# Kernel optimization log

Measured on AMD Instinct MI355X. Metric: run time of the kernel, lower is better.

Reference implementation:

```python
import jax, jax.numpy as jnp
import numpy as np

TIME_SHIFT_OFFSET = 288
NOTE_OFF_OFFSET = 128
VELOCITY_OFFSET = 256
MAX_REL_POS = 25
MAX_REL_TIME = 200
MAX_REL_PITCH = 128


def _last_true_pos(flag):
    # flag: (B,T) bool -> (B,T) index of most recent True at or before each position, -1 if none
    B, T = flag.shape
    pos = jnp.where(flag, jnp.arange(T)[None, :], -1)
    return jax.lax.cummax(pos, axis=1)


def time_rel_idx(tok):
    # Faithful vectorization of Head.relative_time index computation.
    B, T = tok.shape
    is_t = tok >= TIME_SHIFT_OFFSET
    vals = jnp.where(is_t, tok - TIME_SHIFT_OFFSET, 0)
    abs_t = (jnp.cumsum(vals, axis=1) + 1).astype(jnp.float32)
    last = _last_true_pos(is_t)
    cur = jnp.where(last >= 0, jnp.take_along_axis(abs_t, jnp.maximum(last, 0), axis=1), jnp.nan)
    prop = jnp.round(cur / 10.0)  # (B,T), NaN before first time token
    dist = prop[:, None, :] - prop[:, :, None]  # [b,i,j] = prop[j]-prop[i]
    idx = jnp.clip(dist, -MAX_REL_TIME, MAX_REL_TIME) + MAX_REL_TIME
    return jnp.where(jnp.isnan(idx), 0.0, idx).astype(jnp.int32)  # (B,T,T)


def pitch_rel_idx(tok):
    # Per the reference loop, note values are also written one step ahead (i-1,i,i+1),
    # so position j ends up with the note value known after step min(j+1, T-1).
    B, T = tok.shape
    is_n = tok < VELOCITY_OFFSET
    vals = (jnp.where(tok >= NOTE_OFF_OFFSET, tok - NOTE_OFF_OFFSET, tok) + 1).astype(jnp.float32)
    last = _last_true_pos(is_n)
    ff = jnp.where(last >= 0, jnp.take_along_axis(vals, jnp.maximum(last, 0), axis=1), jnp.nan)
    prop = ff[:, jnp.minimum(jnp.arange(T) + 1, T - 1)]
    dist = prop[:, None, :] - prop[:, :, None]
    idx = jnp.clip(dist, -MAX_REL_PITCH, MAX_REL_PITCH) + MAX_REL_PITCH
    return jnp.where(jnp.isnan(idx), 0.0, idx).astype(jnp.int32)  # (B,T,T)


def setup_inputs() -> dict:
    key = jax.random.key(0)
    ks = jax.random.split(key, 12)
    B, T, C, H = 2, 512, 512, 64
    x = jax.random.normal(ks[0], (B, T, C), dtype=jnp.float32)
    token_batch = jax.random.randint(ks[1], (B, T), 0, 388)
    s = C ** -0.5
    Wk = jax.random.normal(ks[2], (C, H), dtype=jnp.float32) * s
    Wq = jax.random.normal(ks[3], (C, H), dtype=jnp.float32) * s
    Wv = jax.random.normal(ks[4], (C, H), dtype=jnp.float32) * s
    e = 0.02
    Ek_pos = jax.random.normal(ks[5], (2 * MAX_REL_POS + 1, H), dtype=jnp.float32) * e
    Ev_pos = jax.random.normal(ks[6], (2 * MAX_REL_POS + 1, H), dtype=jnp.float32) * e
    Ek_time = jax.random.normal(ks[7], (2 * MAX_REL_TIME + 1, H), dtype=jnp.float32) * e
    Ev_time = jax.random.normal(ks[8], (2 * MAX_REL_TIME + 1, H), dtype=jnp.float32) * e
    Ek_pitch = jax.random.normal(ks[9], (2 * MAX_REL_PITCH + 1, H), dtype=jnp.float32) * e
    Ev_pitch = jax.random.normal(ks[10], (2 * MAX_REL_PITCH + 1, H), dtype=jnp.float32) * e
    return dict(x=x, token_batch=token_batch, Wk=Wk, Wq=Wq, Wv=Wv,
                Ek_pos=Ek_pos, Ev_pos=Ev_pos, Ek_time=Ek_time, Ev_time=Ev_time,
                Ek_pitch=Ek_pitch, Ev_pitch=Ev_pitch)


def reference(x, token_batch, Wk, Wq, Wv, Ek_pos, Ev_pos, Ek_time, Ev_time, Ek_pitch, Ev_pitch):
    B, T, C = x.shape
    q = x @ Wq  # (B,T,H)
    k = x @ Wk
    v = x @ Wv
    wei = jnp.einsum('btc,bsc->bts', q, k) * (C ** -0.5)  # (B,T,T), scaled by n_embd per source
    pos = jnp.arange(T)
    pd = jnp.clip(pos[None, :] - pos[:, None], -MAX_REL_POS, MAX_REL_POS) + MAX_REL_POS  # (T,T)
    tidx = time_rel_idx(token_batch)
    nidx = pitch_rel_idx(token_batch)
    # Note: the source einsums sum the relative embeddings over i as well (btj output).
    wei = wei + jnp.einsum('ijc,btc->btj', Ek_pos[pd], q)
    wei = wei + jnp.einsum('bijc,btc->btj', Ek_time[tidx], q)
    wei = wei + jnp.einsum('bijc,btc->btj', Ek_pitch[nidx], q)
    causal = jnp.tril(jnp.ones((T, T), dtype=bool))
    wei = jnp.where(causal[None], wei, -jnp.inf)
    wei = jax.nn.softmax(wei, axis=-1)  # dropout p=0.0
    out = wei @ v
    out = out + jnp.einsum('ijc,btj->btc', Ev_pos[pd], wei)
    out = out + jnp.einsum('bijc,btj->btc', Ev_time[tidx], wei)
    out = out + jnp.einsum('bijc,btj->btc', Ev_pitch[nidx], wei)
    return out
```

## Files before the change

kernel.cpp:

```cpp
#include <hip/hip_runtime.h>
#include <math.h>

#define B 2
#define T 512
#define C 512
#define H 64

#define SCALE 0.044194173824159216f

static __device__ __forceinline__ float qnan() { return __builtin_nanf(""); }

__global__ __launch_bounds__(64) void scan_kernel(const int* __restrict__ tok,
                                                  float* __restrict__ prop_t,
                                                  float* __restrict__ prop_p,
                                                  int* __restrict__ cntP,
                                                  int* __restrict__ meta,
                                                  float* __restrict__ tval,
                                                  int* __restrict__ tcnt) {
    int b = blockIdx.x;
    int lane = threadIdx.x;
    const int* tb = tok + b * T;

    __shared__ int tks[T];
    __shared__ float ptv[T];
    __shared__ float ff[T];
    __shared__ int hist[129];
    __shared__ int cnts[520];
    __shared__ int nanPc;

    for (int i = lane; i < T; i += 64) tks[i] = tb[i];
    for (int i = lane; i < 520; i += 64) cnts[i] = 0;
    for (int i = lane; i < 129; i += 64) hist[i] = 0;
    if (lane == 0) nanPc = 0;
    __syncthreads();

    const int p0 = lane * 8;
    unsigned long long lowmask = lane ? ((1ull << lane) - 1ull) : 0ull;

    {
        float lsum[8];
        bool lflag[8];
        float s = 0.f;
        bool f = false;
#pragma unroll
        for (int i = 0; i < 8; ++i) {
            int tk = tks[p0 + i];
            if (tk >= 288) { s += (float)(tk - 288); f = true; }
            lsum[i] = s;
            lflag[i] = f;
        }
        float inc = s;
#pragma unroll
        for (int off = 1; off < 64; off <<= 1) {
            float o = __shfl_up(inc, off);
            if (lane >= off) inc += o;
        }
        float ex = inc - s;
        unsigned long long fmask = __ballot(f);
        bool exf = (fmask & lowmask) != 0ull;
#pragma unroll
        for (int i = 0; i < 8; ++i) {
            bool have = exf | lflag[i];
            float outv = have ? rintf((ex + lsum[i] + 1.0f) / 10.0f) : qnan();
            prop_t[b * T + p0 + i] = outv;
            ptv[p0 + i] = outv;
        }
    }

    {
        float lval[8];
        bool lvalid[8];
        float cv = 0.f;
        bool cvd = false;
#pragma unroll
        for (int i = 0; i < 8; ++i) {
            int tk = tks[p0 + i];
            if (tk < 256) {
                cv = (float)((tk >= 128 ? tk - 128 : tk) + 1);
                cvd = true;
            }
            lval[i] = cv;
            lvalid[i] = cvd;
        }
        unsigned long long vmask = __ballot(cvd);
        unsigned long long lower = vmask & lowmask;
        bool exvd = lower != 0ull;
        int src = 63 - __clzll(lower | 1ull);
        float exv = __shfl(cv, src);
#pragma unroll
        for (int i = 0; i < 8; ++i) {
            bool hv = exvd | lvalid[i];
            float fv = lvalid[i] ? lval[i] : exv;
            ff[p0 + i] = hv ? fv : qnan();
        }
    }
    __syncthreads();

    for (int i = lane; i < T; i += 64) {
        float v = ff[min(i + 1, T - 1)];
        prop_p[b * T + i] = v;
        if (v == v) atomicAdd(&hist[(int)v - 1], 1);
        else atomicAdd(&nanPc, 1);
    }

    int lstart[8];
    int lcnt = 0, lnan = 0;
#pragma unroll
    for (int u = 0; u < 8; ++u) {
        int i = p0 + u;
        float cur = ptv[i];
        bool val = (cur == cur);
        bool st = false;
        if (val) {
            if (i == 0) st = true;
            else {
                float pv = ptv[i - 1];
                st = !(pv == pv) || (pv != cur);
            }
        } else lnan++;
        lstart[u] = st;
        lcnt += st;
    }
    int incs = lcnt;
#pragma unroll
    for (int off = 1; off < 64; off <<= 1) {
        int o = __shfl_up(incs, off);
        if (lane >= off) incs += o;
    }
    int base = incs - lcnt;
    int Lruns = __shfl(incs, 63);
    int tn = lnan;
#pragma unroll
    for (int off = 32; off; off >>= 1) tn += __shfl_down(tn, off);
    tn = __shfl(tn, 0);

    int s2 = base;
#pragma unroll
    for (int u = 0; u < 8; ++u) {
        int i = p0 + u;
        float cur = ptv[i];
        if (lstart[u]) { tval[b * 520 + s2] = cur; s2++; }
        if (cur == cur) atomicAdd(&cnts[s2 - 1], 1);
    }
    __syncthreads();

    for (int i = lane; i < Lruns; i += 64) tcnt[b * 520 + i] = cnts[i];
    for (int i = lane; i < 129; i += 64) cntP[b * 129 + i] = hist[i];
    if (lane == 0) {
        meta[b * 4] = Lruns;
        meta[b * 4 + 1] = tn;
        meta[b * 4 + 2] = nanPc;
    }
}

__global__ __launch_bounds__(256) void qkv_kernel(const float* __restrict__ x,
                                                  const float* __restrict__ Wq,
                                                  const float* __restrict__ Wk,
                                                  const float* __restrict__ Wv,
                                                  float* __restrict__ q,
                                                  float* __restrict__ k,
                                                  float* __restrict__ v) {
    int rg = blockIdx.x & 255;
    int m = blockIdx.x >> 8;
    int tid = threadIdx.x;
    int wave = tid >> 6;
    int lane = tid & 63;
    int g = lane >> 4;
    int c4 = lane & 15;

    const float* Wm = (m == 0) ? Wq : ((m == 1) ? Wk : Wv);
    float* Om = (m == 0) ? q : ((m == 1) ? k : v);

    __shared__ float xs[4 * C];
    const float4* xv4 = (const float4*)(x + (size_t)rg * 4 * C);
    float4* xs4 = (float4*)xs;
    xs4[tid] = xv4[tid];
    xs4[tid + 256] = xv4[tid + 256];
    __syncthreads();

    const float4* W4 = (const float4*)Wm;
    const float* xr = xs + wave * C;

    float4 acc = make_float4(0.f, 0.f, 0.f, 0.f);
#pragma unroll 8
    for (int u = 0; u < 128; ++u) {
        int kk = u * 4 + g;
        float4 w4 = W4[kk * 16 + c4];
        float xv = xr[kk];
        acc.x = fmaf(xv, w4.x, acc.x);
        acc.y = fmaf(xv, w4.y, acc.y);
        acc.z = fmaf(xv, w4.z, acc.z);
        acc.w = fmaf(xv, w4.w, acc.w);
    }

#pragma unroll
    for (int mask = 16; mask <= 32; mask <<= 1) {
        acc.x += __shfl_xor(acc.x, mask);
        acc.y += __shfl_xor(acc.y, mask);
        acc.z += __shfl_xor(acc.z, mask);
        acc.w += __shfl_xor(acc.w, mask);
    }

    if (g == 0) {
        float4* orow = (float4*)(Om + (size_t)(rg * 4 + wave) * H);
        orow[c4] = acc;
    }
}

__global__ __launch_bounds__(256) void relsum_kernel(
    const float* __restrict__ prop_t, const float* __restrict__ prop_p,
    const int* __restrict__ cntP, const int* __restrict__ meta,
    const float* __restrict__ tval, const int* __restrict__ tcnt,
    const float* __restrict__ Ek_pos, const float* __restrict__ Ev_pos,
    const float* __restrict__ Ek_time, const float* __restrict__ Ev_time,
    const float* __restrict__ Ek_pitch, const float* __restrict__ Ev_pitch,
    float* __restrict__ k, float* __restrict__ v) {
    int b = blockIdx.x >> 9;
    int j = blockIdx.x & 511;
    int tid = threadIdx.x;
    int wave = tid >> 6;
    int c = tid & 63;

    __shared__ float tvL[520];
    __shared__ int tcL[520];
    __shared__ int cpL[129];
    __shared__ float redK[256];
    __shared__ float redV[256];

    int L = meta[b * 4];
    int nanT = meta[b * 4 + 1];
    int nanP = meta[b * 4 + 2];
    for (int i = tid; i < L; i += 256) {
        tvL[i] = tval[b * 520 + i];
        tcL[i] = tcnt[b * 520 + i];
    }
    if (tid < 129) cpL[tid] = cntP[b * 129 + tid];
    __syncthreads();

    float pjt = prop_t[b * T + j];
    float pjp = prop_p[b * T + j];

    float aK = 0.f, aV = 0.f;

    int NE = 130 + L + 1;
    for (int e = wave; e < NE; e += 4) {
        int idx, cnt;
        const float* EK;
        const float* EV;
        if (e < 130) {
            EK = Ek_pitch; EV = Ev_pitch;
            if (e == 129) { idx = 0; cnt = nanP; }
            else {
                cnt = cpL[e];
                float dv = pjp - (float)(e + 1);
                idx = (dv != dv) ? 0 : (int)dv + 128;
            }
        } else {
            EK = Ek_time; EV = Ev_time;
            int r = e - 130;
            if (r == L) { idx = 0; cnt = nanT; }
            else {
                cnt = tcL[r];
                float dt = pjt - tvL[r];
                idx = (dt != dt) ? 0 : (int)fminf(fmaxf(dt, -200.f), 200.f) + 200;
            }
        }
        if (cnt) {
            float fc = (float)cnt;
            aK = fmaf(fc, EK[idx * H + c], aK);
            aV = fmaf(fc, EV[idx * H + c], aV);
        }
    }

    int lo = max(-25, j - (T - 1));
    int hi = min(25, j);
    for (int d = lo + wave; d <= hi; d += 4) {
        aK += Ek_pos[(d + 25) * H + c];
        aV += Ev_pos[(d + 25) * H + c];
    }
    if (wave == 0) {
        float c50 = (float)max(j - 25, 0);
        float c0 = (float)max((T - 26) - j, 0);
        aK = fmaf(c50, Ek_pos[50 * H + c], aK);
        aK = fmaf(c0, Ek_pos[0 * H + c], aK);
        aV = fmaf(c50, Ev_pos[50 * H + c], aV);
        aV = fmaf(c0, Ev_pos[0 * H + c], aV);
    }

    redK[tid] = aK;
    redV[tid] = aV;
    __syncthreads();

    if (tid < 64) {
        float sK = redK[tid] + redK[64 + tid] + redK[128 + tid] + redK[192 + tid];
        float sV = redV[tid] + redV[64 + tid] + redV[128 + tid] + redV[192 + tid];
        size_t o = (size_t)blockIdx.x * H + tid;
        k[o] = SCALE * k[o] + sK;
        v[o] = v[o] + sV;
    }
}

__global__ __launch_bounds__(256) void attn_kernel(const float* __restrict__ q,
                                                   const float* __restrict__ kp,
                                                   const float* __restrict__ vp,
                                                   float* __restrict__ out) {
    int b = blockIdx.x >> 7;
    int g = blockIdx.x & 127;
    int tid = threadIdx.x;
    int wave = tid >> 6;
    int lane = tid & 63;

    int t = (wave < 2) ? (2 * g + wave) : (511 - 2 * g - (wave - 2));
    int ns = t + 1;

    __shared__ float kt[64 * 65];
    __shared__ float vt[64 * 64];
    __shared__ float qs[4][64];
    __shared__ float pS[4][64];

    qs[wave][lane] = q[((size_t)b * T + t) * H + lane];

    const float* kb = kp + (size_t)b * T * H;
    const float* vb = vp + (size_t)b * T * H;
    int ntiles = (512 - 2 * g + 63) / 64;

    float m = -INFINITY;
    float l = 0.f;
    float acc = 0.f;

    for (int it = 0; it < ntiles; ++it) {
        int s0 = it * 64;

#pragma unroll
        for (int i = 0; i < 4; ++i) {
            int f = i * 256 + tid;
            int r = f >> 4;
            int c0 = (f & 15) << 2;
            int sr = min(s0 + r, T - 1);
            const float4 kv = *(const float4*)(kb + (size_t)sr * H + c0);
            const float4 vv = *(const float4*)(vb + (size_t)sr * H + c0);
            kt[r * 65 + c0 + 0] = kv.x;
            kt[r * 65 + c0 + 1] = kv.y;
            kt[r * 65 + c0 + 2] = kv.z;
            kt[r * 65 + c0 + 3] = kv.w;
            *(float4*)(vt + r * 64 + c0) = vv;
        }
        __syncthreads();

        if (s0 < ns) {
            int s = s0 + lane;
            float sc = -INFINITY;
            if (s < ns) {
                float d = 0.f;
                const float* kr = kt + lane * 65;
                const float* qw = qs[wave];
#pragma unroll
                for (int c = 0; c < 64; ++c) d = fmaf(qw[c], kr[c], d);
                sc = d;
            }
            float mt = sc;
#pragma unroll
            for (int off = 32; off; off >>= 1) mt = fmaxf(mt, __shfl_xor(mt, off));
            float mnew = fmaxf(m, mt);
            float alpha = __expf(m - mnew);
            float p = (s < ns) ? __expf(sc - mnew) : 0.f;
            l = l * alpha + p;
            pS[wave][lane] = p;
            m = mnew;

            float a = 0.f;
            int smax = min(64, ns - s0);
            for (int ss = 0; ss < smax; ++ss)
                a = fmaf(pS[wave][ss], vt[ss * 64 + lane], a);
            acc = acc * alpha + a;
        }
        __syncthreads();
    }

    float lt = l;
#pragma unroll
    for (int off = 32; off; off >>= 1) lt += __shfl_xor(lt, off);

    out[((size_t)b * T + t) * H + lane] = acc / lt;
}

extern "C" void kernel_launch(void* const* d_in, const int* in_sizes, int n_in,
                              void* d_out, int out_size, void* d_ws, size_t ws_size,
                              hipStream_t stream) {
    const float* x        = (const float*)d_in[0];
    const int*   tok      = (const int*)d_in[1];
    const float* Wk       = (const float*)d_in[2];
    const float* Wq       = (const float*)d_in[3];
    const float* Wv       = (const float*)d_in[4];
    const float* Ek_pos   = (const float*)d_in[5];
    const float* Ev_pos   = (const float*)d_in[6];
    const float* Ek_time  = (const float*)d_in[7];
    const float* Ev_time  = (const float*)d_in[8];
    const float* Ek_pitch = (const float*)d_in[9];
    const float* Ev_pitch = (const float*)d_in[10];
    float* out = (float*)d_out;

    float* ws = (float*)d_ws;
    float* q      = ws;
    float* k      = q + B * T * H;
    float* v      = k + B * T * H;
    float* prop_t = v + B * T * H;
    float* prop_p = prop_t + B * T;
    int*   cntP   = (int*)(prop_p + B * T);
    int*   meta   = cntP + B * 129;
    float* tval   = (float*)(meta + B * 4);
    int*   tcnt   = (int*)(tval + B * 520);

    scan_kernel<<<B, 64, 0, stream>>>(tok, prop_t, prop_p, cntP, meta, tval, tcnt);
    qkv_kernel<<<3 * 256, 256, 0, stream>>>(x, Wq, Wk, Wv, q, k, v);
    relsum_kernel<<<B * T, 256, 0, stream>>>(prop_t, prop_p, cntP, meta, tval, tcnt,
                                             Ek_pos, Ev_pos, Ek_time, Ev_time,
                                             Ek_pitch, Ev_pitch, k, v);
    attn_kernel<<<B * 128, 256, 0, stream>>>(q, k, v, out);
}
```

Baseline: 137.2 us.

## Register-block QKV projection, split relsum loops, and add ILP accumulators in attention

The QKV kernel now has each wave compute four rows at once, so every weight load is reused four times, and it launches a quarter as many blocks. The relsum kernel splits the mixed pitch/time loop into two separate loops with simpler index math and fewer branches. The attention kernel's dot-product and PV accumulations use four independent accumulators to break serial FMA dependency chains. In exchange, register pressure and shared memory per QKV block go up, fewer QKV blocks may leave parts of the GPU idle, and the changed summation order gives slightly different floating-point results.

New measurement: 131.0 us. 4.5% less time.

```diff
diff --git a/kernel.cpp b/kernel.cpp
--- a/kernel.cpp
+++ b/kernel.cpp
@@ -160,8 +160,8 @@
                                                   float* __restrict__ q,
                                                   float* __restrict__ k,
                                                   float* __restrict__ v) {
-    int rg = blockIdx.x & 255;
-    int m = blockIdx.x >> 8;
+    int rg = blockIdx.x & 63;
+    int m = blockIdx.x >> 6;
     int tid = threadIdx.x;
     int wave = tid >> 6;
     int lane = tid & 63;
@@ -171,39 +171,54 @@
     const float* Wm = (m == 0) ? Wq : ((m == 1) ? Wk : Wv);
     float* Om = (m == 0) ? q : ((m == 1) ? k : v);
 
-    __shared__ float xs[4 * C];
-    const float4* xv4 = (const float4*)(x + (size_t)rg * 4 * C);
+    __shared__ float xs[16 * C];
+    const float4* xv4 = (const float4*)(x + (size_t)rg * 16 * C);
     float4* xs4 = (float4*)xs;
-    xs4[tid] = xv4[tid];
-    xs4[tid + 256] = xv4[tid + 256];
+#pragma unroll
+    for (int i = 0; i < 8; ++i) xs4[tid + 256 * i] = xv4[tid + 256 * i];
     __syncthreads();
 
     const float4* W4 = (const float4*)Wm;
-    const float* xr = xs + wave * C;
-
-    float4 acc = make_float4(0.f, 0.f, 0.f, 0.f);
-#pragma unroll 8
+    const float* xr = xs + (wave * 4) * C;
+
+    float4 a0 = make_float4(0.f, 0.f, 0.f, 0.f);
+    float4 a1 = a0, a2 = a0, a3 = a0;
+#pragma unroll 4
     for (int u = 0; u < 128; ++u) {
         int kk = u * 4 + g;
         float4 w4 = W4[kk * 16 + c4];
-        float xv = xr[kk];
-        acc.x = fmaf(xv, w4.x, acc.x);
-        acc.y = fmaf(xv, w4.y, acc.y);
-        acc.z = fmaf(xv, w4.z, acc.z);
-        acc.w = fmaf(xv, w4.w, acc.w);
+        float x0 = xr[kk];
+        float x1 = xr[C + kk];
+        float x2 = xr[2 * C + kk];
+        float x3 = xr[3 * C + kk];
+        a0.x = fmaf(x0, w4.x, a0.x); a0.y = fmaf(x0, w4.y, a0.y);
+        a0.z = fmaf(x0, w4.z, a0.z); a0.w = fmaf(x0, w4.w, a0.w);
+        a1.x = fmaf(x1, w4.x, a1.x); a1.y = fmaf(x1, w4.y, a1.y);
+        a1.z = fmaf(x1, w4.z, a1.z); a1.w = fmaf(x1, w4.w, a1.w);
+        a2.x = fmaf(x2, w4.x, a2.x); a2.y = fmaf(x2, w4.y, a2.y);
+        a2.z = fmaf(x2, w4.z, a2.z); a2.w = fmaf(x2, w4.w, a2.w);
+        a3.x = fmaf(x3, w4.x, a3.x); a3.y = fmaf(x3, w4.y, a3.y);
+        a3.z = fmaf(x3, w4.z, a3.z); a3.w = fmaf(x3, w4.w, a3.w);
     }
 
 #pragma unroll
     for (int mask = 16; mask <= 32; mask <<= 1) {
-        acc.x += __shfl_xor(acc.x, mask);
-        acc.y += __shfl_xor(acc.y, mask);
-        acc.z += __shfl_xor(acc.z, mask);
-        acc.w += __shfl_xor(acc.w, mask);
+        a0.x += __shfl_xor(a0.x, mask); a0.y += __shfl_xor(a0.y, mask);
+        a0.z += __shfl_xor(a0.z, mask); a0.w += __shfl_xor(a0.w, mask);
+        a1.x += __shfl_xor(a1.x, mask); a1.y += __shfl_xor(a1.y, mask);
+        a1.z += __shfl_xor(a1.z, mask); a1.w += __shfl_xor(a1.w, mask);
+        a2.x += __shfl_xor(a2.x, mask); a2.y += __shfl_xor(a2.y, mask);
+        a2.z += __shfl_xor(a2.z, mask); a2.w += __shfl_xor(a2.w, mask);
+        a3.x += __shfl_xor(a3.x, mask); a3.y += __shfl_xor(a3.y, mask);
+        a3.z += __shfl_xor(a3.z, mask); a3.w += __shfl_xor(a3.w, mask);
     }
 
     if (g == 0) {
-        float4* orow = (float4*)(Om + (size_t)(rg * 4 + wave) * H);
-        orow[c4] = acc;
+        size_t row0 = (size_t)(rg * 16 + wave * 4);
+        ((float4*)(Om + (row0 + 0) * H))[c4] = a0;
+        ((float4*)(Om + (row0 + 1) * H))[c4] = a1;
+        ((float4*)(Om + (row0 + 2) * H))[c4] = a2;
+        ((float4*)(Om + (row0 + 3) * H))[c4] = a3;
     }
 }
 
@@ -223,7 +238,7 @@
 
     __shared__ float tvL[520];
     __shared__ int tcL[520];
-    __shared__ int cpL[129];
+    __shared__ int cpL[132];
     __shared__ float redK[256];
     __shared__ float redV[256];
 
@@ -235,41 +250,46 @@
         tcL[i] = tcnt[b * 520 + i];
     }
     if (tid < 129) cpL[tid] = cntP[b * 129 + tid];
+    else if (tid < 132) cpL[tid] = 0;
     __syncthreads();
 
     float pjt = prop_t[b * T + j];
     float pjp = prop_p[b * T + j];
+    bool pvalid = (pjp == pjp);
+    int ipjp = pvalid ? (int)pjp : 0;
 
     float aK = 0.f, aV = 0.f;
 
-    int NE = 130 + L + 1;
-    for (int e = wave; e < NE; e += 4) {
-        int idx, cnt;
-        const float* EK;
-        const float* EV;
-        if (e < 130) {
-            EK = Ek_pitch; EV = Ev_pitch;
-            if (e == 129) { idx = 0; cnt = nanP; }
-            else {
-                cnt = cpL[e];
-                float dv = pjp - (float)(e + 1);
-                idx = (dv != dv) ? 0 : (int)dv + 128;
-            }
-        } else {
-            EK = Ek_time; EV = Ev_time;
-            int r = e - 130;
-            if (r == L) { idx = 0; cnt = nanT; }
-            else {
-                cnt = tcL[r];
-                float dt = pjt - tvL[r];
-                idx = (dt != dt) ? 0 : (int)fminf(fmaxf(dt, -200.f), 200.f) + 200;
-            }
-        }
+#pragma unroll 3
+    for (int i = 0; i < 33; ++i) {
+        int e = wave + i * 4;
+        int cnt = cpL[e];
         if (cnt) {
+            int idx = pvalid ? (ipjp + 127 - e) : 0;
             float fc = (float)cnt;
-            aK = fmaf(fc, EK[idx * H + c], aK);
-            aV = fmaf(fc, EV[idx * H + c], aV);
-        }
+            aK = fmaf(fc, Ek_pitch[idx * H + c], aK);
+            aV = fmaf(fc, Ev_pitch[idx * H + c], aV);
+        }
+    }
+    if (wave == 3 && nanP) {
+        float fc = (float)nanP;
+        aK = fmaf(fc, Ek_pitch[c], aK);
+        aV = fmaf(fc, Ev_pitch[c], aV);
+    }
+
+#pragma unroll 2
+    for (int r = wave; r < L; r += 4) {
+        int cnt = tcL[r];
+        float dt = pjt - tvL[r];
+        int idx = (dt != dt) ? 0 : (int)fminf(fmaxf(dt, -200.f), 200.f) + 200;
+        float fc = (float)cnt;
+        aK = fmaf(fc, Ek_time[idx * H + c], aK);
+        aV = fmaf(fc, Ev_time[idx * H + c], aV);
+    }
+    if (wave == 1 && nanT) {
+        float fc = (float)nanT;
+        aK = fmaf(fc, Ek_time[c], aK);
+        aV = fmaf(fc, Ev_time[c], aV);
     }
 
     int lo = max(-25, j - (T - 1));
@@ -351,12 +371,17 @@
             int s = s0 + lane;
             float sc = -INFINITY;
             if (s < ns) {
-                float d = 0.f;
                 const float* kr = kt + lane * 65;
                 const float* qw = qs[wave];
-#pragma unroll
-                for (int c = 0; c < 64; ++c) d = fmaf(qw[c], kr[c], d);
-                sc = d;
+                float d0 = 0.f, d1 = 0.f, d2 = 0.f, d3 = 0.f;
+#pragma unroll
+                for (int c = 0; c < 64; c += 4) {
+                    d0 = fmaf(qw[c + 0], kr[c + 0], d0);
+                    d1 = fmaf(qw[c + 1], kr[c + 1], d1);
+                    d2 = fmaf(qw[c + 2], kr[c + 2], d2);
+                    d3 = fmaf(qw[c + 3], kr[c + 3], d3);
+                }
+                sc = (d0 + d1) + (d2 + d3);
             }
             float mt = sc;
 #pragma unroll
@@ -368,11 +393,19 @@
             pS[wave][lane] = p;
             m = mnew;
 
-            float a = 0.f;
+            float a0 = 0.f, a1 = 0.f, a2 = 0.f, a3 = 0.f;
             int smax = min(64, ns - s0);
-            for (int ss = 0; ss < smax; ++ss)
-                a = fmaf(pS[wave][ss], vt[ss * 64 + lane], a);
-            acc = acc * alpha + a;
+            const float* pw = pS[wave];
+            int ss = 0;
+            for (; ss + 4 <= smax; ss += 4) {
+                a0 = fmaf(pw[ss + 0], vt[(ss + 0) * 64 + lane], a0);
+                a1 = fmaf(pw[ss + 1], vt[(ss + 1) * 64 + lane], a1);
+                a2 = fmaf(pw[ss + 2], vt[(ss + 2) * 64 + lane], a2);
+                a3 = fmaf(pw[ss + 3], vt[(ss + 3) * 64 + lane], a3);
+            }
+            for (; ss < smax; ++ss)
+                a0 = fmaf(pw[ss], vt[ss * 64 + lane], a0);
+            acc = acc * alpha + ((a0 + a1) + (a2 + a3));
         }
         __syncthreads();
     }
@@ -412,7 +445,7 @@
     int*   tcnt   = (int*)(tval + B * 520);
 
     scan_kernel<<<B, 64, 0, stream>>>(tok, prop_t, prop_p, cntP, meta, tval, tcnt);
-    qkv_kernel<<<3 * 256, 256, 0, stream>>>(x, Wq, Wk, Wv, q, k, v);
+    qkv_kernel<<<3 * 64, 256, 0, stream>>>(x, Wq, Wk, Wv, q, k, v);
     relsum_kernel<<<B * T, 256, 0, stream>>>(prop_t, prop_p, cntP, meta, tval, tcnt,
                                              Ek_pos, Ev_pos, Ek_time, Ev_time,
                                              Ek_pitch, Ev_pitch, k, v);
```
